# Kernel optimization log

Measured on AMD Instinct MI355X. Metric: run time of the kernel, lower is better.

## Reference

```python
import jax, jax.numpy as jnp
import numpy as np

NUM_HEADS = 12


def setup_inputs() -> dict:
    key = jax.random.key(0)
    k1, k2, k3, k4 = jax.random.split(key, 4)
    B, N, C = 8, 1024, 768
    x = jax.random.normal(k1, (B, N, C), dtype=jnp.float32)
    w_qkv = jax.random.normal(k2, (3 * C, C), dtype=jnp.float32) * 0.02
    w_proj = jax.random.normal(k3, (C, C), dtype=jnp.float32) * 0.02
    b_proj = jax.random.normal(k4, (C,), dtype=jnp.float32) * 0.02
    return {"x": x, "w_qkv": w_qkv, "w_proj": w_proj, "b_proj": b_proj}


def reference(x, w_qkv, w_proj, b_proj):
    B, N, C = x.shape
    H = NUM_HEADS
    D = C // H
    scale = D ** -0.5
    # qkv projection (HMQLinear with quant=False is a plain linear, bias=False)
    qkv = jnp.einsum('bnc,oc->bno', x, w_qkv)          # [B,N,3C]
    qkv = qkv.reshape(B, N, 3, H, D).transpose(2, 0, 3, 1, 4)  # [3,B,H,N,D]
    q, k, v = qkv[0], qkv[1], qkv[2]
    # HMQMulQK (passthrough matmul), scale applied after QK^T as in source
    attn = jnp.einsum('bhqd,bhkd->bhqk', q, k) * scale  # [B,H,N,N]
    attn = jax.nn.softmax(attn, axis=-1)                # HMQSoftmax
    out = jnp.einsum('bhqk,bhkd->bhqd', attn, v)        # HMQMulSV
    out = out.transpose(0, 2, 1, 3).reshape(B, N, C)
    # output projection (HMQLinear, default bias=True)
    return jnp.einsum('bnc,oc->bno', out, w_proj) + b_proj
```

## Files before the change

### kernel.cpp

```cpp
#include <hip/hip_runtime.h>
#include <hip/hip_bf16.h>
#include <stdint.h>

typedef __attribute__((ext_vector_type(8))) short short8;
typedef __attribute__((ext_vector_type(4))) float f32x4;
typedef __attribute__((ext_vector_type(16))) float f32x16;
typedef __attribute__((ext_vector_type(4))) unsigned short us4;

#define AS1 __attribute__((address_space(1)))
#define AS3 __attribute__((address_space(3)))

__device__ inline unsigned short f2bf(float f) {
    unsigned int u = __float_as_uint(f);
    u += 0x7FFFu + ((u >> 16) & 1u);
    return (unsigned short)(u >> 16);
}

__device__ inline unsigned int cvtpk(float lo, float hi) {
    unsigned int r;
    asm("v_cvt_pk_bf16_f32 %0, %1, %2" : "=v"(r) : "v"(lo), "v"(hi));
    return r;
}

__device__ inline void pl32swap(unsigned int& a, unsigned int& b) {
    asm volatile("v_permlane32_swap_b32 %0, %1" : "+v"(a), "+v"(b));
}

__device__ inline float fexp2(float x) {
#if __has_builtin(__builtin_amdgcn_exp2f)
    return __builtin_amdgcn_exp2f(x);
#else
    return exp2f(x);
#endif
}

#define VMW(N) asm volatile("s_waitcnt vmcnt(" #N ")" ::: "memory")
#define BARR() __builtin_amdgcn_s_barrier()

__global__ void cvt_all(const float* __restrict__ x, const float* __restrict__ wq,
                        const float* __restrict__ wp,
                        unsigned short* __restrict__ xb,
                        unsigned short* __restrict__ wqb,
                        unsigned short* __restrict__ wpb) {
    const int X4 = 1572864, Q4 = 442368;
    int i = blockIdx.x * blockDim.x + threadIdx.x;
    const float* src; unsigned short* dst; int j;
    if (i < X4) { src = x; dst = xb; j = i; }
    else if (i < X4 + Q4) { src = wq; dst = wqb; j = i - X4; }
    else { src = wp; dst = wpb; j = i - X4 - Q4; }
    float4 v = ((const float4*)src)[j];
    us4 o;
    o.x = f2bf(v.x); o.y = f2bf(v.y); o.z = f2bf(v.z); o.w = f2bf(v.w);
    ((us4*)dst)[j] = o;
}

#define BM 128
#define BN 128

template<int MODE>
__global__ __launch_bounds__(256)
void gemm_bt(const unsigned short* __restrict__ A,
             const unsigned short* __restrict__ Bm,
             unsigned short* __restrict__ Qo, unsigned short* __restrict__ Ko,
             unsigned short* __restrict__ Vto,
             float* __restrict__ Co, const float* __restrict__ bias,
             int M, int N, int K)
{
    __shared__ __align__(16) unsigned short As[2][BM * 32];
    __shared__ __align__(16) unsigned short Bs[2][BM * 32];
    const int tid = threadIdx.x;
    const int wave = tid >> 6, lane = tid & 63;
    const int tr = blockIdx.x * BM;
    const int tc = blockIdx.y * BN;
    const int wm = wave >> 1, wn = wave & 1;

    f32x4 acc[4][4] = {};

    auto stage = [&](int it, int buf) {
#pragma unroll
        for (int i = 0; i < 2; ++i) {
            int cid = i * 256 + tid;
            int r = cid >> 2, cd = cid & 3;
            int sc = cd ^ (r & 3);
            __builtin_amdgcn_global_load_lds(
                (const AS1 void*)(A + (size_t)(tr + r) * K + it * 32 + sc * 8),
                (AS3 void*)(&As[buf][(i * 256 + wave * 64) * 8]), 16, 0, 0);
            __builtin_amdgcn_global_load_lds(
                (const AS1 void*)(Bm + (size_t)(tc + r) * K + it * 32 + sc * 8),
                (AS3 void*)(&Bs[buf][(i * 256 + wave * 64) * 8]), 16, 0, 0);
        }
    };

    const int nIt = K / 32;
    stage(0, 0);

    for (int it = 0; it < nIt; ++it) {
        const int cur = it & 1;
        if (it + 1 < nIt) { stage(it + 1, cur ^ 1); VMW(4); }
        else              { VMW(0); }
        BARR();

        short8 af[4], bfr[4];
#pragma unroll
        for (int mt = 0; mt < 4; ++mt) {
            int rr = wm * 64 + mt * 16 + (lane & 15);
            af[mt] = *(const short8*)&As[cur][rr * 32 + (((lane >> 4) ^ (rr & 3)) * 8)];
        }
#pragma unroll
        for (int nt = 0; nt < 4; ++nt) {
            int rr = wn * 64 + nt * 16 + (lane & 15);
            bfr[nt] = *(const short8*)&Bs[cur][rr * 32 + (((lane >> 4) ^ (rr & 3)) * 8)];
        }
#pragma unroll
        for (int mt = 0; mt < 4; ++mt)
#pragma unroll
            for (int nt = 0; nt < 4; ++nt)
                acc[mt][nt] = __builtin_amdgcn_mfma_f32_16x16x32_bf16(af[mt], bfr[nt], acc[mt][nt], 0, 0, 0);

        BARR();
    }

    const float QSCALE = 0.18033688011112042f;
#pragma unroll
    for (int mt = 0; mt < 4; ++mt) {
#pragma unroll
        for (int nt = 0; nt < 4; ++nt) {
            int col = tc + wn * 64 + nt * 16 + (lane & 15);
            int row0 = tr + wm * 64 + mt * 16 + (lane >> 4) * 4;
            if constexpr (MODE == 0) {
                int s = (col >= 1536) ? 2 : (col >= 768 ? 1 : 0);
                int rem = col - s * 768;
                int h = rem >> 6, d = rem & 63;
                int b = row0 >> 10, n0 = row0 & 1023;
                int bh = b * 12 + h;
                if (s == 2) {
                    us4 pv;
#pragma unroll
                    for (int r = 0; r < 4; ++r) pv[r] = f2bf(acc[mt][nt][r]);
                    int qd = (n0 >> 2) & 3;
                    int nst = n0 + ((qd == 1) ? 4 : (qd == 2) ? -4 : 0);
                    *(us4*)&Vto[((size_t)bh * 64 + d) * 1024 + nst] = pv;
                } else {
                    unsigned short* dst = (s == 0) ? Qo : Ko;
                    float sc = (s == 0) ? QSCALE : 1.0f;
#pragma unroll
                    for (int r = 0; r < 4; ++r)
                        dst[((size_t)bh * 1024 + n0 + r) * 64 + d] = f2bf(acc[mt][nt][r] * sc);
                }
            } else {
#pragma unroll
                for (int r = 0; r < 4; ++r)
                    Co[(size_t)(row0 + r) * N + col] = acc[mt][nt][r] + bias[col];
            }
        }
    }
}

__global__ __launch_bounds__(256, 3)
void attn_kernel(const unsigned short* __restrict__ Q,
                 const unsigned short* __restrict__ Kg,
                 const unsigned short* __restrict__ Vt,
                 unsigned short* __restrict__ Og)
{
    __shared__ __align__(16) unsigned short KV[2][2][64 * 64];

    const int tid = threadIdx.x;
    const int wave = tid >> 6, lane = tid & 63;
    const int l31 = lane & 31, hi = lane >> 5;
    const int bh = blockIdx.y;
    const int b = bh / 12, h = bh % 12;
    const size_t baseK = (size_t)bh * 1024 * 64;
    const size_t baseV = (size_t)bh * 64 * 1024;
    const int q0 = blockIdx.x * 128 + wave * 32;

    short8 qf[4];
#pragma unroll
    for (int ds = 0; ds < 4; ++ds)
        qf[ds] = *(const short8*)&Q[baseK + (size_t)(q0 + l31) * 64 + ds * 16 + hi * 8];

    f32x16 ot0 = {}, ot1 = {};
    float l = 0.f;

    auto stage = [&](int kt, int buf) {
        const unsigned short* gK = Kg + baseK + (size_t)kt * 64 * 64;
        const unsigned short* gV = Vt + baseV + kt * 64;
#pragma unroll
        for (int i = 0; i < 2; ++i) {
            int c = wave * 128 + i * 64 + lane;
            int r = c >> 3, cc = c & 7;
            int sw = (cc ^ (r & 7)) * 8;
            __builtin_amdgcn_global_load_lds(
                (const AS1 void*)(gK + r * 64 + sw),
                (AS3 void*)(&KV[buf][0][(wave * 128 + i * 64) * 8]), 16, 0, 0);
            __builtin_amdgcn_global_load_lds(
                (const AS1 void*)(gV + (size_t)r * 1024 + sw),
                (AS3 void*)(&KV[buf][1][(wave * 128 + i * 64) * 8]), 16, 0, 0);
        }
    };

    auto rfrag = [&](const unsigned short* s, int row, int cc) -> short8 {
        return *(const short8*)&s[(row * 8 + (cc ^ (row & 7))) * 8];
    };

    auto pack8 = [&](const f32x16& S, int r0) -> short8 {
        union { unsigned int u[4]; short8 s; } fr;
#pragma unroll
        for (int w = 0; w < 4; ++w)
            fr.u[w] = cvtpk(S[r0 + 2 * w], S[r0 + 2 * w + 1]);
        return fr.s;
    };

    stage(0, 0);

    for (int kt = 0; kt < 16; ++kt) {
        const int cur = kt & 1;
        if (kt < 15) { stage(kt + 1, cur ^ 1); VMW(4); }
        else         { VMW(0); }
        BARR();

        f32x16 st0 = {}, st1 = {};
        __builtin_amdgcn_s_setprio(1);
#pragma unroll
        for (int ds = 0; ds < 4; ++ds) {
            short8 k0 = rfrag(KV[cur][0], l31, ds * 2 + hi);
            short8 k1 = rfrag(KV[cur][0], 32 + l31, ds * 2 + hi);
            st0 = __builtin_amdgcn_mfma_f32_32x32x16_bf16(k0, qf[ds], st0, 0, 0, 0);
            st1 = __builtin_amdgcn_mfma_f32_32x32x16_bf16(k1, qf[ds], st1, 0, 0, 0);
        }
        __builtin_amdgcn_s_setprio(0);

        short8 v00 = rfrag(KV[cur][1], l31, 0 + hi);
        short8 v10 = rfrag(KV[cur][1], 32 + l31, 0 + hi);
        short8 v01 = rfrag(KV[cur][1], l31, 2 + hi);
        short8 v11 = rfrag(KV[cur][1], 32 + l31, 2 + hi);

#pragma unroll
        for (int i = 0; i < 16; ++i) st0[i] = fexp2(st0[i]);
        short8 paf0 = pack8(st0, 0);
        short8 paf1 = pack8(st0, 8);

        __builtin_amdgcn_s_setprio(1);
        ot0 = __builtin_amdgcn_mfma_f32_32x32x16_bf16(v00, paf0, ot0, 0, 0, 0);
        ot1 = __builtin_amdgcn_mfma_f32_32x32x16_bf16(v10, paf0, ot1, 0, 0, 0);
        ot0 = __builtin_amdgcn_mfma_f32_32x32x16_bf16(v01, paf1, ot0, 0, 0, 0);
        ot1 = __builtin_amdgcn_mfma_f32_32x32x16_bf16(v11, paf1, ot1, 0, 0, 0);
        __builtin_amdgcn_s_setprio(0);

        short8 v02 = rfrag(KV[cur][1], l31, 4 + hi);
        short8 v12 = rfrag(KV[cur][1], 32 + l31, 4 + hi);
        short8 v03 = rfrag(KV[cur][1], l31, 6 + hi);
        short8 v13 = rfrag(KV[cur][1], 32 + l31, 6 + hi);
#pragma unroll
        for (int i = 0; i < 16; ++i) st1[i] = fexp2(st1[i]);
        short8 paf2 = pack8(st1, 0);
        short8 paf3 = pack8(st1, 8);

        __builtin_amdgcn_s_setprio(1);
        ot0 = __builtin_amdgcn_mfma_f32_32x32x16_bf16(v02, paf2, ot0, 0, 0, 0);
        ot1 = __builtin_amdgcn_mfma_f32_32x32x16_bf16(v12, paf2, ot1, 0, 0, 0);
        ot0 = __builtin_amdgcn_mfma_f32_32x32x16_bf16(v03, paf3, ot0, 0, 0, 0);
        ot1 = __builtin_amdgcn_mfma_f32_32x32x16_bf16(v13, paf3, ot1, 0, 0, 0);
        __builtin_amdgcn_s_setprio(0);

        float su[8];
#pragma unroll
        for (int i = 0; i < 8; ++i)
            su[i] = (st0[2 * i] + st0[2 * i + 1]) + (st1[2 * i] + st1[2 * i + 1]);
#pragma unroll
        for (int s = 4; s > 0; s >>= 1)
#pragma unroll
            for (int i = 0; i < 4; ++i)
                if (i < s) su[i] += su[i + s];
        l += su[0];

        BARR();
    }

    {
        unsigned int pu = __float_as_uint(l), pv = pu;
        pl32swap(pu, pv);
        l += __uint_as_float(hi ? pv : pu);
    }

    float inv = 1.f / l;
#pragma unroll
    for (int i = 0; i < 16; ++i) { ot0[i] *= inv; ot1[i] *= inv; }

    unsigned int* ow = (unsigned int*)(&KV[0][0][0]) + wave * 1152;
#pragma unroll
    for (int dt = 0; dt < 2; ++dt)
#pragma unroll
        for (int rp = 0; rp < 8; ++rp) {
            unsigned int w = (dt == 0) ? cvtpk(ot0[2 * rp], ot0[2 * rp + 1])
                                       : cvtpk(ot1[2 * rp], ot1[2 * rp + 1]);
            int wd = dt * 16 + 4 * (rp >> 1) + 2 * hi + (rp & 1);
            ow[l31 * 36 + wd] = w;
        }
#pragma unroll
    for (int i = 0; i < 4; ++i) {
        int c = i * 64 + lane;
        int qr = c >> 3, ch = c & 7;
        short8 vv = *(const short8*)((const unsigned short*)&ow[qr * 36 + ch * 4]);
        *(short8*)&Og[(size_t)(b * 1024 + q0 + qr) * 768 + h * 64 + ch * 8] = vv;
    }
}

extern "C" void kernel_launch(void* const* d_in, const int* in_sizes, int n_in,
                              void* d_out, int out_size, void* d_ws, size_t ws_size,
                              hipStream_t stream) {
    const float* x      = (const float*)d_in[0];
    const float* w_qkv  = (const float*)d_in[1];
    const float* w_proj = (const float*)d_in[2];
    const float* b_proj = (const float*)d_in[3];
    float* out = (float*)d_out;

    const int Bb = 8, Nn = 1024, C = 768;
    const int M = Bb * Nn;
    const size_t XB = (size_t)M * C;
    const size_t WQ = (size_t)3 * C * C;
    const size_t WP = (size_t)C * C;
    const size_t QE = (size_t)96 * 1024 * 64;

    unsigned short* xb  = (unsigned short*)d_ws;
    unsigned short* wqb = xb + XB;
    unsigned short* wpb = wqb + WQ;
    unsigned short* Qb  = wpb + WP;
    unsigned short* Kb  = Qb + QE;
    unsigned short* Vtb = Kb + QE;
    unsigned short* AO  = Vtb + QE;

    cvt_all<<<8448, 256, 0, stream>>>(x, w_qkv, w_proj, xb, wqb, wpb);

    gemm_bt<0><<<dim3(M / BM, (3 * C) / BN), 256, 0, stream>>>(
        xb, wqb, Qb, Kb, Vtb, nullptr, nullptr, M, 3 * C, C);

    attn_kernel<<<dim3(Nn / 128, Bb * 12), 256, 0, stream>>>(Qb, Kb, Vtb, AO);

    gemm_bt<1><<<dim3(M / BM, C / BN), 256, 0, stream>>>(
        AO, wpb, nullptr, nullptr, nullptr, out, b_proj, M, C, C);
}
```

Baseline: 116.1 us.

## Triple-buffer GEMM and attention K/V staging and add XCD-aware block swizzle

Both the GEMM and the attention kernels move from double-buffered to triple-buffered LDS staging with a prefetch distance of two tiles, so each global load has more time to complete behind compute. Launches become 1D grids with an id remap that groups consecutive tiles onto the same XCD (id&7 striding), meant to improve L2 reuse of shared B/K/V tiles. The cost is more LDS per block: 48KB for the attention kernel, which could lower occupancy under its launch bound of 3 blocks.

After: 126.3 us. 1.09x slower.

```diff
diff --git a/kernel.cpp b/kernel.cpp
--- a/kernel.cpp
+++ b/kernel.cpp
@@ -64,14 +64,20 @@
              unsigned short* __restrict__ Qo, unsigned short* __restrict__ Ko,
              unsigned short* __restrict__ Vto,
              float* __restrict__ Co, const float* __restrict__ bias,
-             int M, int N, int K)
+             int M, int N, int K, int nbx)
 {
-    __shared__ __align__(16) unsigned short As[2][BM * 32];
-    __shared__ __align__(16) unsigned short Bs[2][BM * 32];
+    __shared__ __align__(16) unsigned short As[3][BM * 32];
+    __shared__ __align__(16) unsigned short Bs[3][BM * 32];
     const int tid = threadIdx.x;
     const int wave = tid >> 6, lane = tid & 63;
-    const int tr = blockIdx.x * BM;
-    const int tc = blockIdx.y * BN;
+
+    const int nwg = gridDim.x;
+    const int cpx = nwg >> 3;
+    const int id = blockIdx.x;
+    const int swz = (id & 7) * cpx + (id >> 3);
+    const int tr = (swz % nbx) * BM;
+    const int tc = (swz / nbx) * BN;
+
     const int wm = wave >> 1, wn = wave & 1;
 
     f32x4 acc[4][4] = {};
@@ -93,23 +99,25 @@
 
     const int nIt = K / 32;
     stage(0, 0);
+    stage(1, 1);
+    int cb = 0, sb = 2;
 
     for (int it = 0; it < nIt; ++it) {
-        const int cur = it & 1;
-        if (it + 1 < nIt) { stage(it + 1, cur ^ 1); VMW(4); }
-        else              { VMW(0); }
+        if (it + 2 < nIt)      { stage(it + 2, sb); VMW(8); }
+        else if (it + 1 < nIt) { VMW(4); }
+        else                   { VMW(0); }
         BARR();
 
         short8 af[4], bfr[4];
 #pragma unroll
         for (int mt = 0; mt < 4; ++mt) {
             int rr = wm * 64 + mt * 16 + (lane & 15);
-            af[mt] = *(const short8*)&As[cur][rr * 32 + (((lane >> 4) ^ (rr & 3)) * 8)];
+            af[mt] = *(const short8*)&As[cb][rr * 32 + (((lane >> 4) ^ (rr & 3)) * 8)];
         }
 #pragma unroll
         for (int nt = 0; nt < 4; ++nt) {
             int rr = wn * 64 + nt * 16 + (lane & 15);
-            bfr[nt] = *(const short8*)&Bs[cur][rr * 32 + (((lane >> 4) ^ (rr & 3)) * 8)];
+            bfr[nt] = *(const short8*)&Bs[cb][rr * 32 + (((lane >> 4) ^ (rr & 3)) * 8)];
         }
 #pragma unroll
         for (int mt = 0; mt < 4; ++mt)
@@ -118,6 +126,8 @@
                 acc[mt][nt] = __builtin_amdgcn_mfma_f32_16x16x32_bf16(af[mt], bfr[nt], acc[mt][nt], 0, 0, 0);
 
         BARR();
+        cb = (cb == 2) ? 0 : cb + 1;
+        sb = (sb == 2) ? 0 : sb + 1;
     }
 
     const float QSCALE = 0.18033688011112042f;
@@ -162,16 +172,20 @@
                  const unsigned short* __restrict__ Vt,
                  unsigned short* __restrict__ Og)
 {
-    __shared__ __align__(16) unsigned short KV[2][2][64 * 64];
+    __shared__ __align__(16) unsigned short KV[3][2][64 * 64];
 
     const int tid = threadIdx.x;
     const int wave = tid >> 6, lane = tid & 63;
     const int l31 = lane & 31, hi = lane >> 5;
-    const int bh = blockIdx.y;
+
+    const int id = blockIdx.x;
+    const int swz = (id & 7) * 96 + (id >> 3);
+    const int bh = swz >> 3, qb = swz & 7;
+
     const int b = bh / 12, h = bh % 12;
     const size_t baseK = (size_t)bh * 1024 * 64;
     const size_t baseV = (size_t)bh * 64 * 1024;
-    const int q0 = blockIdx.x * 128 + wave * 32;
+    const int q0 = qb * 128 + wave * 32;
 
     short8 qf[4];
 #pragma unroll
@@ -211,28 +225,30 @@
     };
 
     stage(0, 0);
+    stage(1, 1);
+    int cb = 0, sb = 2;
 
     for (int kt = 0; kt < 16; ++kt) {
-        const int cur = kt & 1;
-        if (kt < 15) { stage(kt + 1, cur ^ 1); VMW(4); }
-        else         { VMW(0); }
+        if (kt < 14)      { stage(kt + 2, sb); VMW(8); }
+        else if (kt < 15) { VMW(4); }
+        else              { VMW(0); }
         BARR();
 
         f32x16 st0 = {}, st1 = {};
         __builtin_amdgcn_s_setprio(1);
 #pragma unroll
         for (int ds = 0; ds < 4; ++ds) {
-            short8 k0 = rfrag(KV[cur][0], l31, ds * 2 + hi);
-            short8 k1 = rfrag(KV[cur][0], 32 + l31, ds * 2 + hi);
+            short8 k0 = rfrag(KV[cb][0], l31, ds * 2 + hi);
+            short8 k1 = rfrag(KV[cb][0], 32 + l31, ds * 2 + hi);
             st0 = __builtin_amdgcn_mfma_f32_32x32x16_bf16(k0, qf[ds], st0, 0, 0, 0);
             st1 = __builtin_amdgcn_mfma_f32_32x32x16_bf16(k1, qf[ds], st1, 0, 0, 0);
         }
         __builtin_amdgcn_s_setprio(0);
 
-        short8 v00 = rfrag(KV[cur][1], l31, 0 + hi);
-        short8 v10 = rfrag(KV[cur][1], 32 + l31, 0 + hi);
-        short8 v01 = rfrag(KV[cur][1], l31, 2 + hi);
-        short8 v11 = rfrag(KV[cur][1], 32 + l31, 2 + hi);
+        short8 v00 = rfrag(KV[cb][1], l31, 0 + hi);
+        short8 v10 = rfrag(KV[cb][1], 32 + l31, 0 + hi);
+        short8 v01 = rfrag(KV[cb][1], l31, 2 + hi);
+        short8 v11 = rfrag(KV[cb][1], 32 + l31, 2 + hi);
 
 #pragma unroll
         for (int i = 0; i < 16; ++i) st0[i] = fexp2(st0[i]);
@@ -246,10 +262,10 @@
         ot1 = __builtin_amdgcn_mfma_f32_32x32x16_bf16(v11, paf1, ot1, 0, 0, 0);
         __builtin_amdgcn_s_setprio(0);
 
-        short8 v02 = rfrag(KV[cur][1], l31, 4 + hi);
-        short8 v12 = rfrag(KV[cur][1], 32 + l31, 4 + hi);
-        short8 v03 = rfrag(KV[cur][1], l31, 6 + hi);
-        short8 v13 = rfrag(KV[cur][1], 32 + l31, 6 + hi);
+        short8 v02 = rfrag(KV[cb][1], l31, 4 + hi);
+        short8 v12 = rfrag(KV[cb][1], 32 + l31, 4 + hi);
+        short8 v03 = rfrag(KV[cb][1], l31, 6 + hi);
+        short8 v13 = rfrag(KV[cb][1], 32 + l31, 6 + hi);
 #pragma unroll
         for (int i = 0; i < 16; ++i) st1[i] = fexp2(st1[i]);
         short8 paf2 = pack8(st1, 0);
@@ -274,6 +290,8 @@
         l += su[0];
 
         BARR();
+        cb = (cb == 2) ? 0 : cb + 1;
+        sb = (sb == 2) ? 0 : sb + 1;
     }
 
     {
@@ -331,11 +349,11 @@
 
     cvt_all<<<8448, 256, 0, stream>>>(x, w_qkv, w_proj, xb, wqb, wpb);
 
-    gemm_bt<0><<<dim3(M / BM, (3 * C) / BN), 256, 0, stream>>>(
-        xb, wqb, Qb, Kb, Vtb, nullptr, nullptr, M, 3 * C, C);
-
-    attn_kernel<<<dim3(Nn / 128, Bb * 12), 256, 0, stream>>>(Qb, Kb, Vtb, AO);
-
-    gemm_bt<1><<<dim3(M / BM, C / BN), 256, 0, stream>>>(
-        AO, wpb, nullptr, nullptr, nullptr, out, b_proj, M, C, C);
-}
+    gemm_bt<0><<<(M / BM) * ((3 * C) / BN), 256, 0, stream>>>(
+        xb, wqb, Qb, Kb, Vtb, nullptr, nullptr, M, 3 * C, C, M / BM);
+
+    attn_kernel<<<768, 256, 0, stream>>>(Qb, Kb, Vtb, AO);
+
+    gemm_bt<1><<<(M / BM) * (C / BN), 256, 0, stream>>>(
+        AO, wpb, nullptr, nullptr, nullptr, out, b_proj, M, C, C, M / BM);
+}
```
